# Optimization experiments

Hardware: AMD Instinct MI355X
Metric: run time of the kernel (lower is better)

The kernel has to match this reference:

```python
import jax, jax.numpy as jnp
import numpy as np

V, E, H, L, T_BLOCK = 50257, 1024, 16, 8, 1024
HS = E // H  # 64
F_ = 4 * E
STD = 0.02


def _ln(x, g, b, eps=1e-5):
    mu = jnp.mean(x, axis=-1, keepdims=True)
    var = jnp.var(x, axis=-1, keepdims=True)
    return (x - mu) * jax.lax.rsqrt(var + eps) * g + b


def setup_inputs() -> dict:
    key = jax.random.key(0)
    ks = jax.random.split(key, 16)
    n = lambda k, shp: (STD * jax.random.normal(k, shp)).astype(jnp.float32)
    inp = {
        "idx": jax.random.randint(ks[0], (4, 1024), 0, V, dtype=jnp.int32).astype(jnp.int64),
        "tok_emb": n(ks[1], (V, E)),
        "pos_emb": n(ks[2], (T_BLOCK, E)),
        "wq": n(ks[3], (L, H, E, HS)),
        "wk": n(ks[4], (L, H, E, HS)),
        "wv": n(ks[5], (L, H, E, HS)),
        "wo": n(ks[6], (L, E, E)),
        "bo": jnp.zeros((L, E), jnp.float32),
        "ln1g": jnp.ones((L, E), jnp.float32),
        "ln1b": jnp.zeros((L, E), jnp.float32),
        "ln2g": jnp.ones((L, E), jnp.float32),
        "ln2b": jnp.zeros((L, E), jnp.float32),
        "w1": n(ks[7], (L, E, F_)),
        "b1": jnp.zeros((L, F_), jnp.float32),
        "w2": n(ks[8], (L, F_, E)),
        "b2": jnp.zeros((L, E), jnp.float32),
        "lnfg": jnp.ones((E,), jnp.float32),
        "lnfb": jnp.zeros((E,), jnp.float32),
    }
    return inp


def reference(idx, tok_emb, pos_emb, wq, wk, wv, wo, bo, ln1g, ln1b,
              ln2g, ln2b, w1, b1, w2, b2, lnfg, lnfb):
    B, T = idx.shape
    x = tok_emb[idx] + pos_emb[:T]  # [B,T,E]
    mask = jnp.tril(jnp.ones((T, T), dtype=bool))  # causal
    scale = HS ** -0.5
    for l in range(L):
        h = _ln(x, ln1g[l], ln1b[l])
        q = jnp.einsum('bte,hed->bhtd', h, wq[l])
        k = jnp.einsum('bte,hed->bhtd', h, wk[l])
        v = jnp.einsum('bte,hed->bhtd', h, wv[l])
        att = jnp.einsum('bhtd,bhsd->bhts', q, k) * scale
        att = jnp.where(mask, att, -jnp.inf)
        att = jax.nn.softmax(att, axis=-1)
        o = jnp.einsum('bhts,bhsd->bhtd', att, v)
        o = o.transpose(0, 2, 1, 3).reshape(B, T, E)  # concat heads
        x = x + o @ wo[l] + bo[l]
        h2 = _ln(x, ln2g[l], ln2b[l])
        x = x + jax.nn.relu(h2 @ w1[l] + b1[l]) @ w2[l] + b2[l]
    x = _ln(x, lnfg, lnfb)
    logits = x @ tok_emb.T  # tied lm_head, no bias
    return logits
```

## Files before the change

### kernel.cpp

```cpp
#include <hip/hip_runtime.h>
#include <cstdint>

#define B_ 4
#define T_ 1024
#define E_ 1024
#define H_ 16
#define HS_ 64
#define L_ 8
#define F_DIM 4096
#define V_ 50257
#define VP2_ 50432

typedef __attribute__((ext_vector_type(8))) short bf16x8;
typedef __attribute__((ext_vector_type(4))) float f32x4;
typedef unsigned short u16;

__device__ inline float b2f(u16 u) {
  unsigned int v = ((unsigned int)u) << 16;
  return __builtin_bit_cast(float, v);
}
__device__ inline u16 f2b(float f) {
  unsigned int u = __builtin_bit_cast(unsigned int, f);
  unsigned int r = (u + 0x7FFFu + ((u >> 16) & 1u)) >> 16;
  return (u16)r;
}

__device__ inline float wave_sum(float v) {
#pragma unroll
  for (int off = 32; off > 0; off >>= 1) v += __shfl_down(v, off);
  return v;
}

#define GLOAD16(gp, lp)                                                        \
  __builtin_amdgcn_global_load_lds(                                            \
      (const __attribute__((address_space(1))) unsigned int*)(gp),             \
      (__attribute__((address_space(3))) unsigned int*)(lp), 16, 0, 0)

__global__ __launch_bounds__(256) void embed_kernel(
    const int* __restrict__ idx, const float* __restrict__ tok,
    const float* __restrict__ pos, float* __restrict__ x) {
  int bt = blockIdx.x;
  int t = bt & (T_ - 1);
  int tid = threadIdx.x;
  int tokid = idx[bt];
  float4 a = reinterpret_cast<const float4*>(tok + (size_t)tokid * E_)[tid];
  float4 p = reinterpret_cast<const float4*>(pos + (size_t)t * E_)[tid];
  float4 r = make_float4(a.x + p.x, a.y + p.y, a.z + p.z, a.w + p.w);
  reinterpret_cast<float4*>(x + (size_t)bt * E_)[tid] = r;
}

__global__ __launch_bounds__(256) void ln_kernel(
    const float* __restrict__ in, const float* __restrict__ g,
    const float* __restrict__ b, u16* __restrict__ out) {
  int row = blockIdx.x;
  int tid = threadIdx.x;
  const float* xr = in + (size_t)row * E_;
  float4 v = reinterpret_cast<const float4*>(xr)[tid];
  float s = v.x + v.y + v.z + v.w;
  float q = v.x * v.x + v.y * v.y + v.z * v.z + v.w * v.w;
  s = wave_sum(s);
  q = wave_sum(q);
  __shared__ float ls[4], lq[4];
  int wid = tid >> 6;
  if ((tid & 63) == 0) { ls[wid] = s; lq[wid] = q; }
  __syncthreads();
  float st = ls[0] + ls[1] + ls[2] + ls[3];
  float qt = lq[0] + lq[1] + lq[2] + lq[3];
  float mu = st * (1.0f / E_);
  float var = qt * (1.0f / E_) - mu * mu;
  float inv = rsqrtf(var + 1e-5f);
  float4 gg = reinterpret_cast<const float4*>(g)[tid];
  float4 bb = reinterpret_cast<const float4*>(b)[tid];
  ushort4 o4;
  o4.x = f2b((v.x - mu) * inv * gg.x + bb.x);
  o4.y = f2b((v.y - mu) * inv * gg.y + bb.y);
  o4.z = f2b((v.z - mu) * inv * gg.z + bb.z);
  o4.w = f2b((v.w - mu) * inv * gg.w + bb.w);
  reinterpret_cast<ushort4*>(out + (size_t)row * E_)[tid] = o4;
}

__global__ __launch_bounds__(256) void convT_kernel(
    const float* __restrict__ in, u16* __restrict__ out, int K, int N) {
  __shared__ float tile[64][65];
  int n0 = blockIdx.x * 64, k0 = blockIdx.y * 64;
  int tx = threadIdx.x & 63, ty = threadIdx.x >> 6;
#pragma unroll
  for (int r = 0; r < 64; r += 4)
    tile[r + ty][tx] = in[(size_t)(k0 + r + ty) * N + n0 + tx];
  __syncthreads();
#pragma unroll
  for (int r = 0; r < 64; r += 4)
    out[(size_t)(n0 + r + ty) * K + k0 + tx] = f2b(tile[tx][r + ty]);
}

__global__ __launch_bounds__(256) void convQKV_kernel(
    const float* __restrict__ wq, const float* __restrict__ wk,
    const float* __restrict__ wv, u16* __restrict__ out) {
  int src = blockIdx.x >> 4, hh = blockIdx.x & 15, e0 = blockIdx.y * 64;
  const float* w =
      (src == 0 ? wq : (src == 1 ? wk : wv)) + (size_t)hh * E_ * HS_;
  __shared__ float tile[64][65];
  int tx = threadIdx.x & 63, ty = threadIdx.x >> 6;
#pragma unroll
  for (int r = 0; r < 64; r += 4)
    tile[r + ty][tx] = w[(size_t)(e0 + r + ty) * HS_ + tx];
  __syncthreads();
  size_t nb = (size_t)src * 1024 + hh * 64;
#pragma unroll
  for (int r = 0; r < 64; r += 4)
    out[(nb + r + ty) * E_ + e0 + tx] = f2b(tile[tx][r + ty]);
}

__global__ __launch_bounds__(256) void convTok_kernel(
    const float* __restrict__ tok, u16* __restrict__ out) {
  int row = blockIdx.x;
  int tid = threadIdx.x;
  ushort4 o4;
  if (row < V_) {
    float4 v = reinterpret_cast<const float4*>(tok + (size_t)row * E_)[tid];
    o4.x = f2b(v.x); o4.y = f2b(v.y); o4.z = f2b(v.z); o4.w = f2b(v.w);
  } else {
    o4 = make_ushort4(0, 0, 0, 0);
  }
  reinterpret_cast<ushort4*>(out + (size_t)row * E_)[tid] = o4;
}

__global__ __launch_bounds__(256) void vtrans_kernel(
    const u16* __restrict__ qkv, u16* __restrict__ vt) {
  int t0 = blockIdx.x * 64;
  int bh = blockIdx.y;
  int b = bh >> 4, hh = bh & 15;
  __shared__ unsigned int tile[64][65];
  int tx = threadIdx.x & 63, ty = threadIdx.x >> 6;
  const u16* src = qkv + ((size_t)(b * T_ + t0)) * 3072 + 2048 + hh * 64;
#pragma unroll
  for (int r = 0; r < 64; r += 4)
    tile[r + ty][tx] = src[(size_t)(r + ty) * 3072 + tx];
  __syncthreads();
  u16* dst = vt + ((size_t)bh * 64) * 1024 + t0;
#pragma unroll
  for (int r = 0; r < 64; r += 4)
    dst[(size_t)(r + ty) * 1024 + tx] = (u16)tile[tx][r + ty];
}

__global__ __launch_bounds__(512) void gemm8p_kernel(
    const u16* __restrict__ A, int lda, const u16* __restrict__ Bt, int ldb,
    const float* __restrict__ bias, float* __restrict__ Cf,
    u16* __restrict__ Cb, int ldc, int N, int K, int gm, int flags) {
  __shared__ u16 As[2][256 * 64];
  __shared__ u16 Bs[2][256 * 64];

  int nwg = gridDim.x;
  int q8 = nwg >> 3;
  int bid = blockIdx.x;
  int wg = (bid & 7) * q8 + (bid >> 3);
  int m0 = (wg % gm) * 256, n0 = (wg / gm) * 256;

  int tid = threadIdx.x;
  int w = tid >> 6, lane = tid & 63;
  int wr = w >> 2, wc = w & 3;
  int l15 = lane & 15, lg = lane >> 4;
  int swzr = (l15 & 7) << 3;

  int l8 = lane >> 3;
  int swz_e = ((lane & 7) ^ l8) << 3;
  int wq = w & 3, wh = w >> 2;
  const u16* aSrc[4];
  const u16* bSrc[4];
#pragma unroll
  for (int qq = 0; qq < 4; ++qq) {
    aSrc[qq] = A + (size_t)(m0 + wh * 128 + qq * 32 + wq * 8 + l8) * lda;
    bSrc[qq] = Bt + (size_t)(n0 + (w >> 1) * 64 + qq * 16 + (w & 1) * 8 + l8) * ldb;
  }

#define STAGE_A(qq, tt, bb)                                                    \
  GLOAD16(aSrc[qq] + (size_t)(tt) * 64 + swz_e,                                \
          &As[bb][(wh * 128 + (qq) * 32 + wq * 8) * 64])
#define STAGE_B(qq, tt, bb)                                                    \
  GLOAD16(bSrc[qq] + (size_t)(tt) * 64 + swz_e,                                \
          &Bs[bb][((w >> 1) * 64 + (qq) * 16 + (w & 1) * 8) * 64])
#define LDA_OFF(mf, ks) \
  (((wr * 128 + (mf) * 16 + l15) * 64) + ((((ks) * 32) + lg * 8) ^ swzr))
#define LDB_OFF(nf, ks) \
  (((wc * 64 + (nf) * 16 + l15) * 64) + ((((ks) * 32) + lg * 8) ^ swzr))
#define WAITV(n) asm volatile("s_waitcnt vmcnt(" #n ")" ::: "memory")

  f32x4 acc[8][4];
#pragma unroll
  for (int i = 0; i < 8; ++i)
#pragma unroll
    for (int j = 0; j < 4; ++j) acc[i][j] = (f32x4){0.f, 0.f, 0.f, 0.f};

  STAGE_B(0, 0, 0); STAGE_B(1, 0, 0); STAGE_B(2, 0, 0); STAGE_B(3, 0, 0);
  STAGE_A(0, 0, 0); STAGE_A(1, 0, 0); STAGE_A(2, 0, 0); STAGE_A(3, 0, 0);
  WAITV(3);
  __builtin_amdgcn_sched_barrier(0);
  __builtin_amdgcn_s_barrier();
  __builtin_amdgcn_sched_barrier(0);

  int NT = K >> 6;
  bf16x8 bfrag[4][2];
  for (int t = 0; t < NT; ++t) {
    int cur = t & 1, nxt = cur ^ 1;
    bool pf = (t + 1 < NT);
    int t1 = t + 1;
#pragma unroll
    for (int p = 0; p < 4; ++p) {
      bf16x8 a0k0 = *(const bf16x8*)&As[cur][LDA_OFF(2 * p + 0, 0)];
      bf16x8 a0k1 = *(const bf16x8*)&As[cur][LDA_OFF(2 * p + 0, 1)];
      bf16x8 a1k0 = *(const bf16x8*)&As[cur][LDA_OFF(2 * p + 1, 0)];
      bf16x8 a1k1 = *(const bf16x8*)&As[cur][LDA_OFF(2 * p + 1, 1)];
      if (p == 0) {
#pragma unroll
        for (int nf = 0; nf < 4; ++nf) {
          bfrag[nf][0] = *(const bf16x8*)&Bs[cur][LDB_OFF(nf, 0)];
          bfrag[nf][1] = *(const bf16x8*)&Bs[cur][LDB_OFF(nf, 1)];
        }
      }
      if (pf) {
        if (p == 0) { STAGE_B(0, t1, nxt); STAGE_B(1, t1, nxt); }
        else if (p == 1) { STAGE_B(2, t1, nxt); STAGE_B(3, t1, nxt); }
        else if (p == 2) { STAGE_A(0, t1, nxt); STAGE_A(1, t1, nxt); }
        else { STAGE_A(2, t1, nxt); STAGE_A(3, t1, nxt); }
      }
      __builtin_amdgcn_s_barrier();
      asm volatile("s_waitcnt lgkmcnt(0)" ::: "memory");
      __builtin_amdgcn_sched_barrier(0);
      __builtin_amdgcn_s_setprio(1);
#pragma unroll
      for (int nf = 0; nf < 4; ++nf) {
        acc[2 * p + 0][nf] = __builtin_amdgcn_mfma_f32_16x16x32_bf16(
            a0k0, bfrag[nf][0], acc[2 * p + 0][nf], 0, 0, 0);
        acc[2 * p + 0][nf] = __builtin_amdgcn_mfma_f32_16x16x32_bf16(
            a0k1, bfrag[nf][1], acc[2 * p + 0][nf], 0, 0, 0);
        acc[2 * p + 1][nf] = __builtin_amdgcn_mfma_f32_16x16x32_bf16(
            a1k0, bfrag[nf][0], acc[2 * p + 1][nf], 0, 0, 0);
        acc[2 * p + 1][nf] = __builtin_amdgcn_mfma_f32_16x16x32_bf16(
            a1k1, bfrag[nf][1], acc[2 * p + 1][nf], 0, 0, 0);
      }
      __builtin_amdgcn_s_setprio(0);
      if (pf) {
        if (p == 0) WAITV(4);
        else if (p == 1) WAITV(5);
        else if (p == 2) WAITV(6);
        else WAITV(3);
      } else {
        if (p == 0) WAITV(2);
        else if (p == 1) WAITV(1);
        else WAITV(0);
      }
      __builtin_amdgcn_sched_barrier(0);
      __builtin_amdgcn_s_barrier();
      __builtin_amdgcn_sched_barrier(0);
    }
  }

#pragma unroll
  for (int mf = 0; mf < 8; ++mf) {
#pragma unroll
    for (int nf = 0; nf < 4; ++nf) {
      int n = n0 + wc * 64 + nf * 16 + l15;
      if (n < N) {
        float bv = bias ? bias[n] : 0.f;
#pragma unroll
        for (int j = 0; j < 4; ++j) {
          int m = m0 + wr * 128 + mf * 16 + lg * 4 + j;
          float r = acc[mf][nf][j] + bv;
          if (flags & 2) r = fmaxf(r, 0.f);
          if (Cb)
            Cb[(size_t)m * ldc + n] = f2b(r);
          else
            Cf[(size_t)m * ldc + n] = r;
        }
      }
    }
  }
#undef STAGE_A
#undef STAGE_B
#undef LDA_OFF
#undef LDB_OFF
#undef WAITV
}

__global__ __launch_bounds__(256) void mfma_gemm_kernel(
    const u16* __restrict__ A, int lda, const u16* __restrict__ Bt, int ldb,
    const float* __restrict__ bias, float* __restrict__ Cf,
    u16* __restrict__ Cb, int ldc, int N, int K, int flags) {
  __shared__ u16 As[128 * 32];
  __shared__ u16 Bs[128 * 32];
  int m0 = blockIdx.x * 128, n0 = blockIdx.y * 128;
  int tid = threadIdx.x;
  int wave = tid >> 6, lane = tid & 63;
  int wr = wave >> 1, wc = wave & 1;

  f32x4 acc[4][4];
#pragma unroll
  for (int i = 0; i < 4; ++i)
#pragma unroll
    for (int j = 0; j < 4; ++j) acc[i][j] = (f32x4){0.f, 0.f, 0.f, 0.f};

  int c0 = wave * 2, c1 = wave * 2 + 1;
  int sr0 = c0 * 16 + (lane >> 2), sr1 = c1 * 16 + (lane >> 2);
  int sc = (lane & 3) * 8;
  const u16* Ag0 = A + (size_t)(m0 + sr0) * lda + sc;
  const u16* Ag1 = A + (size_t)(m0 + sr1) * lda + sc;
  const u16* Bg0 = Bt + (size_t)(n0 + sr0) * ldb + sc;
  const u16* Bg1 = Bt + (size_t)(n0 + sr1) * ldb + sc;
  u16* lA0 = &As[c0 * 512];
  u16* lA1 = &As[c1 * 512];
  u16* lB0 = &Bs[c0 * 512];
  u16* lB1 = &Bs[c1 * 512];

  int lrow = lane & 15, loct = lane >> 4;
  const int arow0 = (wr * 64 + lrow) * 32 + loct * 8;
  const int brow0 = (wc * 64 + lrow) * 32 + loct * 8;

  for (int k0 = 0; k0 < K; k0 += 32) {
    GLOAD16(Ag0 + k0, lA0);
    GLOAD16(Ag1 + k0, lA1);
    GLOAD16(Bg0 + k0, lB0);
    GLOAD16(Bg1 + k0, lB1);
    __syncthreads();
    bf16x8 af[4], bfr[4];
#pragma unroll
    for (int mf = 0; mf < 4; ++mf)
      af[mf] = *(const bf16x8*)&As[arow0 + mf * 16 * 32];
#pragma unroll
    for (int nf = 0; nf < 4; ++nf)
      bfr[nf] = *(const bf16x8*)&Bs[brow0 + nf * 16 * 32];
#pragma unroll
    for (int mf = 0; mf < 4; ++mf)
#pragma unroll
      for (int nf = 0; nf < 4; ++nf)
        acc[mf][nf] = __builtin_amdgcn_mfma_f32_16x16x32_bf16(
            af[mf], bfr[nf], acc[mf][nf], 0, 0, 0);
    __syncthreads();
  }

  int lq = lane >> 4;
#pragma unroll
  for (int mf = 0; mf < 4; ++mf) {
#pragma unroll
    for (int nf = 0; nf < 4; ++nf) {
      int n = n0 + wc * 64 + nf * 16 + lrow;
      if (n < N) {
        float bv = bias ? bias[n] : 0.f;
#pragma unroll
        for (int j = 0; j < 4; ++j) {
          int m = m0 + wr * 64 + mf * 16 + lq * 4 + j;
          float r = acc[mf][nf][j] + bv;
          if (flags & 1) r += Cf[(size_t)m * ldc + n];
          if (flags & 2) r = fmaxf(r, 0.f);
          if (Cb)
            Cb[(size_t)m * ldc + n] = f2b(r);
          else
            Cf[(size_t)m * ldc + n] = r;
        }
      }
    }
  }
}

__global__ __launch_bounds__(256) void fattn_kernel(
    const u16* __restrict__ qkv, const u16* __restrict__ vt,
    u16* __restrict__ o) {
  int t0 = (gridDim.x - 1 - blockIdx.x) * 64;
  int bh = blockIdx.y;
  int b = bh >> 4, hh = bh & 15;
  int tid = threadIdx.x;
  int w = tid >> 6, lane = tid & 63;
  int c = lane & 15, g = lane >> 4;

  __shared__ u16 Ks[64][72];
  __shared__ u16 Vs[64][72];
  __shared__ u16 Ps[4][16][72];

  const u16* qbase = qkv + (size_t)(b * T_) * 3072 + hh * 64;
  const u16* kbase = qbase + 1024;
  const u16* vbase = vt + (size_t)bh * 64 * 1024;

  bf16x8 qf[2];
  {
    const u16* qrow = qbase + (size_t)(t0 + w * 16 + c) * 3072 + g * 8;
#pragma unroll
    for (int kh = 0; kh < 2; ++kh) {
      bf16x8 tq = *(const bf16x8*)(qrow + kh * 32);
#pragma unroll
      for (int j = 0; j < 8; ++j) tq[j] = (short)f2b(b2f((u16)tq[j]) * 0.125f);
      qf[kh] = tq;
    }
  }

  float m[4] = {-1e30f, -1e30f, -1e30f, -1e30f};
  float l[4] = {0.f, 0.f, 0.f, 0.f};
  f32x4 acc[4];
#pragma unroll
  for (int ds = 0; ds < 4; ++ds) acc[ds] = (f32x4){0.f, 0.f, 0.f, 0.f};

  int tq0 = t0 + w * 16 + g * 4;

  for (int kv0 = 0; kv0 <= t0; kv0 += 64) {
    __syncthreads();
#pragma unroll
    for (int i = tid; i < 512; i += 256) {
      int r = i >> 3, cc = i & 7;
      *(int4*)&Ks[r][cc * 8] =
          *(const int4*)(kbase + (size_t)(kv0 + r) * 3072 + cc * 8);
      *(int4*)&Vs[r][cc * 8] =
          *(const int4*)(vbase + (size_t)r * 1024 + kv0 + cc * 8);
    }
    __syncthreads();

    f32x4 s[4];
#pragma unroll
    for (int ct = 0; ct < 4; ++ct) {
      bf16x8 kf0 = *(const bf16x8*)&Ks[ct * 16 + c][g * 8];
      bf16x8 kf1 = *(const bf16x8*)&Ks[ct * 16 + c][g * 8 + 32];
      s[ct] = (f32x4){0.f, 0.f, 0.f, 0.f};
      s[ct] =
          __builtin_amdgcn_mfma_f32_16x16x32_bf16(qf[0], kf0, s[ct], 0, 0, 0);
      s[ct] =
          __builtin_amdgcn_mfma_f32_16x16x32_bf16(qf[1], kf1, s[ct], 0, 0, 0);
    }
#pragma unroll
    for (int ct = 0; ct < 4; ++ct) {
      int tk = kv0 + ct * 16 + c;
#pragma unroll
      for (int j = 0; j < 4; ++j)
        if (tk > tq0 + j) s[ct][j] = -1e30f;
    }
#pragma unroll
    for (int j = 0; j < 4; ++j) {
      float mt = fmaxf(fmaxf(s[0][j], s[1][j]), fmaxf(s[2][j], s[3][j]));
#pragma unroll
      for (int off = 1; off < 16; off <<= 1)
        mt = fmaxf(mt, __shfl_xor(mt, off));
      float mn = fmaxf(m[j], mt);
      float sc = __expf(m[j] - mn);
      m[j] = mn;
      float rs = 0.f;
#pragma unroll
      for (int ct = 0; ct < 4; ++ct) {
        float p = __expf(s[ct][j] - mn);
        s[ct][j] = p;
        rs += p;
      }
#pragma unroll
      for (int off = 1; off < 16; off <<= 1) rs += __shfl_xor(rs, off);
      l[j] = l[j] * sc + rs;
#pragma unroll
      for (int ds = 0; ds < 4; ++ds) acc[ds][j] *= sc;
    }
#pragma unroll
    for (int ct = 0; ct < 4; ++ct)
#pragma unroll
      for (int j = 0; j < 4; ++j)
        Ps[w][g * 4 + j][ct * 16 + c] = f2b(s[ct][j]);
    bf16x8 pf0 = *(const bf16x8*)&Ps[w][c][g * 8];
    bf16x8 pf1 = *(const bf16x8*)&Ps[w][c][g * 8 + 32];
#pragma unroll
    for (int ds = 0; ds < 4; ++ds) {
      bf16x8 vf0 = *(const bf16x8*)&Vs[ds * 16 + c][g * 8];
      bf16x8 vf1 = *(const bf16x8*)&Vs[ds * 16 + c][g * 8 + 32];
      acc[ds] =
          __builtin_amdgcn_mfma_f32_16x16x32_bf16(pf0, vf0, acc[ds], 0, 0, 0);
      acc[ds] =
          __builtin_amdgcn_mfma_f32_16x16x32_bf16(pf1, vf1, acc[ds], 0, 0, 0);
    }
  }

  float inv[4];
#pragma unroll
  for (int j = 0; j < 4; ++j) inv[j] = 1.0f / l[j];
  u16* orow = o + ((size_t)(b * T_ + tq0)) * E_ + hh * 64;
#pragma unroll
  for (int ds = 0; ds < 4; ++ds)
#pragma unroll
    for (int j = 0; j < 4; ++j)
      orow[(size_t)j * E_ + ds * 16 + c] = f2b(acc[ds][j] * inv[j]);
}

extern "C" void kernel_launch(void* const* d_in, const int* in_sizes, int n_in,
                              void* d_out, int out_size, void* d_ws,
                              size_t ws_size, hipStream_t stream) {
  (void)in_sizes; (void)n_in; (void)out_size; (void)ws_size;
  const int* idx = (const int*)d_in[0];
  const float* tok_emb = (const float*)d_in[1];
  const float* pos_emb = (const float*)d_in[2];
  const float* wq = (const float*)d_in[3];
  const float* wk = (const float*)d_in[4];
  const float* wv = (const float*)d_in[5];
  const float* wo = (const float*)d_in[6];
  const float* bo = (const float*)d_in[7];
  const float* ln1g = (const float*)d_in[8];
  const float* ln1b = (const float*)d_in[9];
  const float* ln2g = (const float*)d_in[10];
  const float* ln2b = (const float*)d_in[11];
  const float* w1 = (const float*)d_in[12];
  const float* b1 = (const float*)d_in[13];
  const float* w2 = (const float*)d_in[14];
  const float* b2 = (const float*)d_in[15];
  const float* lnfg = (const float*)d_in[16];
  const float* lnfb = (const float*)d_in[17];
  float* out = (float*)d_out;
  char* ws = (char*)d_ws;

  u16* h = (u16*)(ws + 0);
  float* x = (float*)(ws + 8388608);
  u16* qkvb = (u16*)(ws + 25165824);
  u16* ob = (u16*)(ws + 50331648);
  u16* ffb = (u16*)(ws + 58720256);
  u16* wqkvT = (u16*)(ws + 92274688);
  u16* woT = (u16*)(ws + 98566144);
  u16* w1T = (u16*)(ws + 100663296);
  u16* w2T = (u16*)(ws + 109051904);
  u16* vtb = (u16*)(ws + 117440512);
  u16* tokb = (u16*)(ws + 8388608);

  embed_kernel<<<B_ * T_, 256, 0, stream>>>(idx, tok_emb, pos_emb, x);

  for (int l = 0; l < L_; ++l) {
    ln_kernel<<<B_ * T_, 256, 0, stream>>>(x, ln1g + l * E_, ln1b + l * E_, h);
    convQKV_kernel<<<dim3(48, 16), 256, 0, stream>>>(
        wq + (size_t)l * H_ * E_ * HS_, wk + (size_t)l * H_ * E_ * HS_,
        wv + (size_t)l * H_ * E_ * HS_, wqkvT);
    gemm8p_kernel<<<16 * 12, 512, 0, stream>>>(
        h, E_, wqkvT, E_, nullptr, nullptr, qkvb, 3072, 3072, E_, 16, 0);
    vtrans_kernel<<<dim3(16, 64), 256, 0, stream>>>(qkvb, vtb);
    fattn_kernel<<<dim3(16, 64), 256, 0, stream>>>(qkvb, vtb, ob);
    convT_kernel<<<dim3(16, 16), 256, 0, stream>>>(
        wo + (size_t)l * E_ * E_, woT, E_, E_);
    mfma_gemm_kernel<<<dim3(32, 8), 256, 0, stream>>>(
        ob, E_, woT, E_, bo + (size_t)l * E_, x, nullptr, E_, E_, E_, 1);
    ln_kernel<<<B_ * T_, 256, 0, stream>>>(x, ln2g + l * E_, ln2b + l * E_, h);
    convT_kernel<<<dim3(64, 16), 256, 0, stream>>>(
        w1 + (size_t)l * E_ * F_DIM, w1T, E_, F_DIM);
    gemm8p_kernel<<<16 * 16, 512, 0, stream>>>(
        h, E_, w1T, E_, b1 + (size_t)l * F_DIM, nullptr, ffb, F_DIM, F_DIM,
        E_, 16, 2);
    convT_kernel<<<dim3(16, 64), 256, 0, stream>>>(
        w2 + (size_t)l * F_DIM * E_, w2T, F_DIM, E_);
    mfma_gemm_kernel<<<dim3(32, 8), 256, 0, stream>>>(
        ffb, F_DIM, w2T, F_DIM, b2 + (size_t)l * E_, x, nullptr, E_, E_,
        F_DIM, 1);
  }

  ln_kernel<<<B_ * T_, 256, 0, stream>>>(x, lnfg, lnfb, h);
  convTok_kernel<<<VP2_, 256, 0, stream>>>(tok_emb, tokb);
  gemm8p_kernel<<<16 * (VP2_ / 256), 512, 0, stream>>>(
      h, E_, tokb, E_, nullptr, out, nullptr, V_, V_, E_, 16, 0);
}
```

Measured before the change: 3.332 ms.

## Use persistent-M lm_head GEMM so each block sweeps many M tiles per N strip

Replaces the lm_head GEMM launch with a new kernel in which each block owns one 256-wide vocab strip and loops over 16 row tiles of 128 (half of M). The aim is better L2 locality for the large tied embedding weight and fewer blocks. The new kernel drops software pipelining and still reloads the B tile each k-step, so per-iteration latency exposure may rise. Far fewer blocks (394) could also underfill the GPU.

```diff
diff --git a/kernel.cpp b/kernel.cpp
--- a/kernel.cpp
+++ b/kernel.cpp
@@ -361,6 +361,86 @@
   }
 }
 
+__global__ __launch_bounds__(512) void gemmpm_kernel(
+    const u16* __restrict__ A, int lda, const u16* __restrict__ Bt, int ldb,
+    float* __restrict__ Cf, int ldc, int N, int K) {
+  __shared__ u16 As[128 * 64];
+  __shared__ u16 Bs[256 * 64];
+  int nt = blockIdx.x >> 1;
+  int mh = blockIdx.x & 1;
+  int n0 = nt * 256;
+
+  int tid = threadIdx.x;
+  int w = tid >> 6, lane = tid & 63;
+  int wr = w >> 2, wc = w & 3;
+  int l15 = lane & 15, lg = lane >> 4;
+  int l8 = lane >> 3;
+  int swz_e = ((lane & 7) ^ l8) << 3;
+  int swzr = (l15 & 7) << 3;
+
+  const u16* bSrc[4];
+#pragma unroll
+  for (int g = 0; g < 4; ++g)
+    bSrc[g] = Bt + (size_t)(n0 + g * 64 + w * 8 + l8) * ldb + swz_e;
+
+  for (int mi = 0; mi < 16; ++mi) {
+    int m0 = mh * 2048 + mi * 128;
+    const u16* aSrc0 = A + (size_t)(m0 + w * 8 + l8) * lda + swz_e;
+    const u16* aSrc1 = aSrc0 + (size_t)64 * lda;
+
+    f32x4 acc[4][4];
+#pragma unroll
+    for (int i = 0; i < 4; ++i)
+#pragma unroll
+      for (int j = 0; j < 4; ++j) acc[i][j] = (f32x4){0.f, 0.f, 0.f, 0.f};
+
+    for (int k0 = 0; k0 < K; k0 += 64) {
+      GLOAD16(aSrc0 + k0, &As[(w * 8) * 64]);
+      GLOAD16(aSrc1 + k0, &As[(64 + w * 8) * 64]);
+#pragma unroll
+      for (int g = 0; g < 4; ++g)
+        GLOAD16(bSrc[g] + k0, &Bs[(g * 64 + w * 8) * 64]);
+      __syncthreads();
+      bf16x8 af[4][2];
+#pragma unroll
+      for (int mf = 0; mf < 4; ++mf) {
+        int ro = (wr * 64 + mf * 16 + l15) * 64;
+        af[mf][0] = *(const bf16x8*)&As[ro + ((lg * 8) ^ swzr)];
+        af[mf][1] = *(const bf16x8*)&As[ro + ((32 + lg * 8) ^ swzr)];
+      }
+#pragma unroll
+      for (int nf = 0; nf < 4; ++nf) {
+        int ro = (wc * 64 + nf * 16 + l15) * 64;
+        bf16x8 b0 = *(const bf16x8*)&Bs[ro + ((lg * 8) ^ swzr)];
+        bf16x8 b1 = *(const bf16x8*)&Bs[ro + ((32 + lg * 8) ^ swzr)];
+#pragma unroll
+        for (int mf = 0; mf < 4; ++mf) {
+          acc[mf][nf] = __builtin_amdgcn_mfma_f32_16x16x32_bf16(
+              af[mf][0], b0, acc[mf][nf], 0, 0, 0);
+          acc[mf][nf] = __builtin_amdgcn_mfma_f32_16x16x32_bf16(
+              af[mf][1], b1, acc[mf][nf], 0, 0, 0);
+        }
+      }
+      __syncthreads();
+    }
+
+#pragma unroll
+    for (int mf = 0; mf < 4; ++mf) {
+#pragma unroll
+      for (int nf = 0; nf < 4; ++nf) {
+        int n = n0 + wc * 64 + nf * 16 + l15;
+        if (n < N) {
+#pragma unroll
+          for (int j = 0; j < 4; ++j) {
+            int m = m0 + wr * 64 + mf * 16 + lg * 4 + j;
+            Cf[(size_t)m * ldc + n] = acc[mf][nf][j];
+          }
+        }
+      }
+    }
+  }
+}
+
 __global__ __launch_bounds__(256) void fattn_kernel(
     const u16* __restrict__ qkv, const u16* __restrict__ vt,
     u16* __restrict__ o) {
@@ -547,6 +627,6 @@
 
   ln_kernel<<<B_ * T_, 256, 0, stream>>>(x, lnfg, lnfb, h);
   convTok_kernel<<<VP2_, 256, 0, stream>>>(tok_emb, tokb);
-  gemm8p_kernel<<<16 * (VP2_ / 256), 512, 0, stream>>>(
-      h, E_, tokb, E_, nullptr, out, nullptr, V_, V_, E_, 16, 0);
-}
+  gemmpm_kernel<<<2 * (VP2_ / 256), 512, 0, stream>>>(
+      h, E_, tokb, E_, out, V_, V_, E_);
+}
```

New measurement: 3.428 ms. +2.9%, slower.

## Add B-stationary lm_head GEMM keeping full vocab slice resident in LDS

Applied to the files above, without the earlier changes.

Replaces the generic tiled GEMM for the final logits projection with a new kernel. Each block loads a 64-column slice of the token embedding matrix (all of K=1024) into LDS once, then streams all 4096 rows of activations in 128-row tiles with double-buffered async loads. The aim is to read the large vocabulary weight matrix from global memory only once instead of once per M tile. In exchange it uses roughly 160KB of LDS per block, which limits occupancy to one block per CU. The grid shrinks to about 788 blocks, each doing a long serial loop with only 16x64 outputs per wave, so MFMA throughput per wave may be low.

```diff
diff --git a/kernel.cpp b/kernel.cpp
--- a/kernel.cpp
+++ b/kernel.cpp
@@ -361,6 +361,88 @@
   }
 }
 
+__global__ __launch_bounds__(512) void gemmbl_kernel(
+    const u16* __restrict__ A, int lda, const u16* __restrict__ Bt, int ldb,
+    float* __restrict__ Cf, int ldc, int N, int K) {
+  __shared__ u16 Bl[16 * 64 * 64];
+  __shared__ u16 Al[2][128 * 64];
+  int n0 = blockIdx.x * 64;
+
+  int tid = threadIdx.x;
+  int w = tid >> 6, lane = tid & 63;
+  int l15 = lane & 15, lg = lane >> 4;
+  int l8 = lane >> 3;
+  int swz_e = ((lane & 7) ^ l8) << 3;
+  int swzr = (l15 & 7) << 3;
+
+#define WAITV(n) asm volatile("s_waitcnt vmcnt(" #n ")" ::: "memory")
+
+  {
+    const u16* bSrc = Bt + (size_t)(n0 + w * 8 + l8) * ldb + swz_e;
+#pragma unroll
+    for (int s = 0; s < 16; ++s)
+      GLOAD16(bSrc + s * 64, &Bl[s * 4096 + w * 512]);
+  }
+  GLOAD16(A + (size_t)(w * 8 + l8) * lda + swz_e, &Al[0][(w * 8) * 64]);
+  GLOAD16(A + (size_t)(64 + w * 8 + l8) * lda + swz_e,
+          &Al[0][(64 + w * 8) * 64]);
+  WAITV(0);
+  __builtin_amdgcn_s_barrier();
+
+  for (int mi = 0; mi < 32; ++mi) {
+    int m0 = mi * 128;
+    f32x4 acc[4];
+#pragma unroll
+    for (int nf = 0; nf < 4; ++nf) acc[nf] = (f32x4){0.f, 0.f, 0.f, 0.f};
+
+    for (int kt = 0; kt < 16; ++kt) {
+      int cb = kt & 1;
+      if (!(mi == 31 && kt == 15)) {
+        int nkt = kt + 1, nmi = mi;
+        if (nkt == 16) { nkt = 0; nmi = mi + 1; }
+        int nm0 = nmi * 128;
+        GLOAD16(A + (size_t)(nm0 + w * 8 + l8) * lda + nkt * 64 + swz_e,
+                &Al[cb ^ 1][(w * 8) * 64]);
+        GLOAD16(A + (size_t)(nm0 + 64 + w * 8 + l8) * lda + nkt * 64 + swz_e,
+                &Al[cb ^ 1][(64 + w * 8) * 64]);
+      }
+      bf16x8 af0 = *(const bf16x8*)&Al[cb][(w * 16 + l15) * 64 +
+                                          ((lg * 8) ^ swzr)];
+      bf16x8 af1 = *(const bf16x8*)&Al[cb][(w * 16 + l15) * 64 +
+                                          ((32 + lg * 8) ^ swzr)];
+      int bbase = kt * 4096;
+      __builtin_amdgcn_s_setprio(1);
+#pragma unroll
+      for (int nf = 0; nf < 4; ++nf) {
+        bf16x8 b0 = *(const bf16x8*)&Bl[bbase + (nf * 16 + l15) * 64 +
+                                        ((lg * 8) ^ swzr)];
+        bf16x8 b1 = *(const bf16x8*)&Bl[bbase + (nf * 16 + l15) * 64 +
+                                        ((32 + lg * 8) ^ swzr)];
+        acc[nf] = __builtin_amdgcn_mfma_f32_16x16x32_bf16(af0, b0, acc[nf],
+                                                          0, 0, 0);
+        acc[nf] = __builtin_amdgcn_mfma_f32_16x16x32_bf16(af1, b1, acc[nf],
+                                                          0, 0, 0);
+      }
+      __builtin_amdgcn_s_setprio(0);
+      WAITV(0);
+      __builtin_amdgcn_s_barrier();
+    }
+
+#pragma unroll
+    for (int nf = 0; nf < 4; ++nf) {
+      int n = n0 + nf * 16 + l15;
+      if (n < N) {
+#pragma unroll
+        for (int j = 0; j < 4; ++j) {
+          int m = m0 + w * 16 + lg * 4 + j;
+          Cf[(size_t)m * ldc + n] = acc[nf][j];
+        }
+      }
+    }
+  }
+#undef WAITV
+}
+
 __global__ __launch_bounds__(256) void fattn_kernel(
     const u16* __restrict__ qkv, const u16* __restrict__ vt,
     u16* __restrict__ o) {
@@ -547,6 +629,6 @@
 
   ln_kernel<<<B_ * T_, 256, 0, stream>>>(x, lnfg, lnfb, h);
   convTok_kernel<<<VP2_, 256, 0, stream>>>(tok_emb, tokb);
-  gemm8p_kernel<<<16 * (VP2_ / 256), 512, 0, stream>>>(
-      h, E_, tokb, E_, nullptr, out, nullptr, V_, V_, E_, 16, 0);
-}
+  gemmbl_kernel<<<VP2_ / 64, 512, 0, stream>>>(
+      h, E_, tokb, E_, out, V_, V_, E_);
+}
```

After: 4.385 ms. 31.6% more time.
